# Optimization experiments

Hardware: AMD Instinct MI355X
Metric: run time of the kernel (lower is better)

The kernel has to match this reference:

```python
import jax, jax.numpy as jnp
import numpy as np

B, Nres, TOP_K, NUM_RBF = 2, 2048, 30, 16
MAX_REL = 32  # positional clip range -> 2*32+2 = 66 classes


def _gather_nodes(nodes, idx):
    # nodes: [B, N, ...], idx: [B, N, K] -> [B, N, K, ...]
    return jax.vmap(lambda n, i: n[i])(nodes, idx)


def _rbf(D):
    # D: [..., ] -> [..., NUM_RBF]; mu in [2, 22], sigma = 20/16
    mu = jnp.linspace(2.0, 22.0, NUM_RBF)
    sigma = (22.0 - 2.0) / NUM_RBF
    return jnp.exp(-(((D[..., None] - mu) / sigma) ** 2))


def setup_inputs() -> dict:
    key = jax.random.key(0)
    ks = jax.random.split(key, 4)
    X = jax.random.normal(ks[0], (B, Nres, 4, 3), dtype=jnp.float32) * 3.0
    mask = jnp.ones((B, Nres), dtype=jnp.float32)
    residue_idx = jnp.broadcast_to(jnp.arange(Nres, dtype=jnp.int32)[None], (B, Nres))
    chain_labels = jnp.zeros((B, Nres), dtype=jnp.int32)
    w_pos = jax.random.normal(ks[1], (66, 16), dtype=jnp.float32) * 0.05
    b_pos = jax.random.normal(ks[2], (16,), dtype=jnp.float32) * 0.05
    w_edge = jax.random.normal(ks[3], (416, 128), dtype=jnp.float32) * 0.05
    ln_gamma = jnp.ones((128,), dtype=jnp.float32)
    ln_beta = jnp.zeros((128,), dtype=jnp.float32)
    return dict(X=X, mask=mask, residue_idx=residue_idx, chain_labels=chain_labels,
                w_pos=w_pos, b_pos=b_pos, w_edge=w_edge, ln_gamma=ln_gamma, ln_beta=ln_beta)


def reference(X, mask, residue_idx, chain_labels, w_pos, b_pos, w_edge, ln_gamma, ln_beta):
    # virtual C-beta from N, C, Ca (atom order in X: N=0, C=1, Ca=2, O=3)
    b = X[:, :, 2, :] - X[:, :, 0, :]
    c = X[:, :, 1, :] - X[:, :, 2, :]
    a = jnp.cross(b, c)
    Cb = -0.58273431 * a + 0.56802827 * b - 0.54067466 * c + X[:, :, 2, :]
    N_, C, Ca, O = X[:, :, 0, :], X[:, :, 1, :], X[:, :, 2, :], X[:, :, 3, :]

    # masked kNN on C atoms (ProteinFeatures._dist)
    m2 = mask[:, None, :] * mask[:, :, None]                       # [B,N,N]
    dX = C[:, None, :, :] - C[:, :, None, :]
    D = m2 * jnp.sqrt(jnp.sum(dX ** 2, -1) + 1e-6)
    D_max = jnp.max(D, -1, keepdims=True)
    D_adj = D + (1.0 - m2) * D_max
    neg, E_idx = jax.lax.top_k(-D_adj, TOP_K)                      # smallest-k
    D_neighbors = -neg                                             # [B,N,K]

    # 25-channel RBF features; gather neighbor coords instead of NxN per pair
    atoms = jnp.stack([N_, Ca, Cb, C, O], 0)                       # [5,B,N,3]
    gathered = jax.vmap(lambda A: _gather_nodes(A, E_idx))(atoms)  # [5,B,N,K,3]
    # pair order follows torch source: NN,CaCa,CbCb,CN,CCa,CCb,NCa,NCb,CbCa,
    # NC,CaC,CbC,CaN,CbN,CaCb,OO,CO,OC,NO,ON,CbO,OCa,OCb,CaO  (0=N,1=Ca,2=Cb,3=C,4=O)
    pa = jnp.array([0, 1, 2, 3, 3, 3, 0, 0, 2, 0, 1, 2, 1, 2, 1, 4, 3, 4, 0, 4, 2, 4, 4, 1])
    pb = jnp.array([0, 1, 2, 0, 1, 2, 1, 2, 1, 3, 3, 3, 0, 0, 2, 4, 4, 3, 4, 0, 4, 1, 2, 4])
    A_sel = atoms[pa]                                              # [24,B,N,3]
    Bn_sel = gathered[pb]                                          # [24,B,N,K,3]
    Dp = jnp.sqrt(jnp.sum((A_sel[:, :, :, None, :] - Bn_sel) ** 2, -1) + 1e-6)
    RBF_all = jnp.concatenate([_rbf(D_neighbors)[None], _rbf(Dp)], 0)  # [25,B,N,K,16]
    RBF_all = jnp.moveaxis(RBF_all, 0, 3).reshape(B, Nres, TOP_K, 25 * NUM_RBF)

    # positional encodings over gathered offsets / chain match
    offset = residue_idx[:, :, None] - _gather_nodes(residue_idx, E_idx)   # [B,N,K]
    E_chains = (chain_labels[:, :, None] == _gather_nodes(chain_labels, E_idx)).astype(jnp.int32)
    d = jnp.clip(offset + MAX_REL, 0, 2 * MAX_REL) * E_chains + (1 - E_chains) * (2 * MAX_REL + 1)
    E_pos = w_pos[d] + b_pos                                       # one_hot @ W == gather

    # edge embedding + layernorm
    E = jnp.concatenate([E_pos, RBF_all], -1) @ w_edge             # [B,N,K,128]
    mu = E.mean(-1, keepdims=True)
    var = E.var(-1, keepdims=True)
    E = (E - mu) / jnp.sqrt(var + 1e-5) * ln_gamma + ln_beta
    return E, E_idx
```

## Files before the change

kernel.cpp:

```cpp
#include <hip/hip_runtime.h>
#include <hip/hip_bf16.h>
#include <stdint.h>

#define BB    2
#define NRES  2048
#define TOPK  30
#define NRBF  16
#define NFEAT 416
#define NCH   128
#define NKT   13

typedef __attribute__((ext_vector_type(8))) short bf16x8;
typedef __attribute__((ext_vector_type(4))) float f32x4;

__constant__ int c_pa[24] = {0,1,2,3,3,3,0,0,2,0,1,2,1,2,1,4,3,4,0,4,2,4,4,1};
__constant__ int c_pb[24] = {0,1,2,0,1,2,1,2,1,3,3,3,0,0,2,4,4,3,4,0,4,1,2,4};

static __device__ __forceinline__ unsigned short f2bf(float x) {
  __hip_bfloat16 h = __float2bfloat16(x);
  return *reinterpret_cast<unsigned short*>(&h);
}
static __device__ __forceinline__ unsigned pack2(float lo, float hi) {
  return (unsigned)f2bf(lo) | ((unsigned)f2bf(hi) << 16);
}

__global__ __launch_bounds__(256) void prep_kernel(const float* __restrict__ X,
                                                   const float* __restrict__ w_edge,
                                                   float* __restrict__ atoms,
                                                   float4* __restrict__ Cpk,
                                                   unsigned short* __restrict__ wB) {
  if (blockIdx.x < 16) {
    int id = blockIdx.x * 256 + threadIdx.x;
    const float* x = X + (size_t)id * 12;
    float nx = x[0], ny = x[1], nz = x[2];
    float cx = x[3], cy = x[4], cz = x[5];
    float ax = x[6], ay = x[7], az = x[8];
    float ox = x[9], oy = x[10], oz = x[11];
    float bx = ax - nx, by = ay - ny, bz = az - nz;
    float ccx = cx - ax, ccy = cy - ay, ccz = cz - az;
    float crx = by * ccz - bz * ccy;
    float cry = bz * ccx - bx * ccz;
    float crz = bx * ccy - by * ccx;
    float cbx = -0.58273431f * crx + 0.56802827f * bx - 0.54067466f * ccx + ax;
    float cby = -0.58273431f * cry + 0.56802827f * by - 0.54067466f * ccy + ay;
    float cbz = -0.58273431f * crz + 0.56802827f * bz - 0.54067466f * ccz + az;
    float* r = atoms + (size_t)id * 16;
    r[0] = nx;  r[1] = ny;  r[2] = nz;
    r[3] = ax;  r[4] = ay;  r[5] = az;
    r[6] = cbx; r[7] = cby; r[8] = cbz;
    r[9] = cx;  r[10] = cy; r[11] = cz;
    r[12] = ox; r[13] = oy; r[14] = oz;
    r[15] = 0.f;
    Cpk[id] = make_float4(cx, cy, cz, 0.f);
  } else {
    int id = (blockIdx.x - 16) * 256 + threadIdx.x;
    if (id >= NFEAT * NCH) return;
    int j    = id & 7;
    int lane = (id >> 3) & 63;
    int nt   = (id >> 9) & 7;
    int kt   = id >> 12;
    int col  = nt * 16 + (lane & 15);
    int k    = kt * 32 + ((lane >> 4) << 3) + j;
    wB[id] = f2bf(w_edge[(size_t)k * NCH + col]);
  }
}

__global__ __launch_bounds__(256) void topk_kernel(const float4* __restrict__ Cpk,
                                                   int* __restrict__ eidx,
                                                   float* __restrict__ dn,
                                                   float* __restrict__ outI) {
  int tid = threadIdx.x;
  int lane = tid & 63;
  int bi = blockIdx.x * 4 + (tid >> 6);
  int b = bi >> 11;
  int i = bi & (NRES - 1);
  const float4* Cb = Cpk + (size_t)b * NRES;
  float4 ci = Cb[i];

  unsigned long long key[4][8];
  unsigned long long sub[4];
#pragma unroll
  for (int g = 0; g < 4; ++g) {
    sub[g] = ~0ull;
#pragma unroll
    for (int s = 0; s < 8; ++s) {
      int j = lane + 64 * (g * 8 + s);
      float4 cj = Cb[j];
      float dx = cj.x - ci.x, dy = cj.y - ci.y, dz = cj.z - ci.z;
      float sm = __fadd_rn(__fadd_rn(__fadd_rn(__fmul_rn(dx, dx), __fmul_rn(dy, dy)),
                                     __fmul_rn(dz, dz)), 1e-6f);
      float d = sqrtf(sm);
      key[g][s] = ((unsigned long long)__float_as_uint(d) << 32) | (unsigned)j;
      if (key[g][s] < sub[g]) sub[g] = key[g][s];
    }
  }

  for (int k = 0; k < TOPK; ++k) {
    unsigned long long m01 = sub[0] < sub[1] ? sub[0] : sub[1];
    unsigned long long m23 = sub[2] < sub[3] ? sub[2] : sub[3];
    unsigned long long gm = m01 < m23 ? m01 : m23;
#pragma unroll
    for (int off = 32; off; off >>= 1) {
      unsigned long long o = __shfl_xor(gm, off, 64);
      if (o < gm) gm = o;
    }
    if (lane == 0) {
      int idx = (int)(unsigned)(gm & 0xffffffffu);
      eidx[(size_t)bi * TOPK + k] = idx;
      dn[(size_t)bi * TOPK + k] = __uint_as_float((unsigned)(gm >> 32));
      outI[(size_t)bi * TOPK + k] = (float)idx;
    }
#pragma unroll
    for (int g = 0; g < 4; ++g) {
      if (sub[g] == gm) {
        sub[g] = ~0ull;
#pragma unroll
        for (int s = 0; s < 8; ++s) {
          if (key[g][s] == gm) key[g][s] = ~0ull;
          if (key[g][s] < sub[g]) sub[g] = key[g][s];
        }
      }
    }
  }
}

__global__ __launch_bounds__(256) void edge_mfma_kernel(
    const float* __restrict__ atoms, const int* __restrict__ eidx_g,
    const float* __restrict__ dn_g, const int* __restrict__ ridx,
    const int* __restrict__ chain, const float* __restrict__ w_pos,
    const float* __restrict__ b_pos, const unsigned short* __restrict__ wB,
    const float* __restrict__ gamma, const float* __restrict__ beta,
    float* __restrict__ outE) {
  __shared__ __align__(16) unsigned fa[NKT * 4 * 32 * 4];
  __shared__ float nat[TOPK][16];
  __shared__ float iat[16];
  __shared__ float dn_s[TOPK];
  __shared__ int   dsel[TOPK];
  __shared__ float2 lnp[32][4];

  int tid = threadIdx.x;
  int bi = blockIdx.x;
  int b = bi >> 11;

  if (tid < TOPK) {
    dn_s[tid] = dn_g[(size_t)bi * TOPK + tid];
    int j = eidx_g[(size_t)bi * TOPK + tid];
    int off = ridx[bi] - ridx[b * NRES + j];
    int ec = (chain[bi] == chain[b * NRES + j]) ? 1 : 0;
    int d = off + 32; d = d < 0 ? 0 : (d > 64 ? 64 : d);
    dsel[tid] = ec ? d : 65;
  }
  if (tid >= 64 && tid < 80) iat[tid - 64] = atoms[(size_t)bi * 16 + (tid - 64)];
  for (int idx = tid; idx < TOPK * 16; idx += 256) {
    int e = idx >> 4, f = idx & 15;
    nat[e][f] = atoms[((size_t)(b * NRES) + eidx_g[(size_t)bi * TOPK + e]) * 16 + f];
  }
  for (int idx = tid; idx < NKT * 4 * 2 * 4; idx += 256) {
    int kt4q = idx >> 3, row = 30 + ((idx >> 2) & 1), jw = idx & 3;
    fa[(kt4q * 32 + row) * 4 + jw] = 0u;
  }
  __syncthreads();

  if (tid < TOPK * 8) {
    int e = tid >> 3, u = tid & 7;
    int q = u >> 2, jw = u & 3;
    int f0 = u * 2, ds = dsel[e];
    float v0 = w_pos[ds * 16 + f0] + b_pos[f0];
    float v1 = w_pos[ds * 16 + f0 + 1] + b_pos[f0 + 1];
    fa[((q * 32) + e) * 4 + jw] = pack2(v0, v1);
  }
  for (int idx = tid; idx < TOPK * 25; idx += 256) {
    int e = idx / 25, g = idx - e * 25;
    float d;
    if (g == 0) {
      d = dn_s[e];
    } else {
      int qq = g - 1;
      const float* A  = &iat[c_pa[qq] * 3];
      const float* Bv = &nat[e][c_pb[qq] * 3];
      float dx = A[0] - Bv[0], dy = A[1] - Bv[1], dz = A[2] - Bv[2];
      d = sqrtf(dx * dx + dy * dy + dz * dz + 1e-6f);
    }
    unsigned tmp[8];
#pragma unroll
    for (int j = 0; j < 8; ++j) {
      float mu0 = 2.0f + (float)(2 * j) * (20.0f / 15.0f);
      float mu1 = 2.0f + (float)(2 * j + 1) * (20.0f / 15.0f);
      float t0 = (d - mu0) * 0.8f, t1 = (d - mu1) * 0.8f;
      tmp[j] = pack2(__expf(-t0 * t0), __expf(-t1 * t1));
    }
    int u0 = 8 + 8 * g;
    int kt = u0 >> 4, q0 = (u0 >> 2) & 3;
    unsigned* dst0 = &fa[(((kt * 4 + q0) * 32) + e) * 4];
    unsigned* dst1 = &fa[(((kt * 4 + q0 + 1) * 32) + e) * 4];
    *(uint4*)dst0 = make_uint4(tmp[0], tmp[1], tmp[2], tmp[3]);
    *(uint4*)dst1 = make_uint4(tmp[4], tmp[5], tmp[6], tmp[7]);
  }
  __syncthreads();

  int nq = tid >> 6, lane = tid & 63;
  int q = lane >> 4;
  int ccol = lane & 15;
  const uint4* faq = ((const uint4*)fa) + q * 32;
  const bf16x8* wBv = (const bf16x8*)wB;

  union AV { uint4 u4; bf16x8 v; };
  AV a0[2], a1[2];
  bf16x8 b0[3], b1[3];
#pragma unroll
  for (int t = 0; t < 3; ++t) {
    b0[t] = wBv[((size_t)(t * 8) + nq * 2 + 0) * 64 + lane];
    b1[t] = wBv[((size_t)(t * 8) + nq * 2 + 1) * 64 + lane];
  }
#pragma unroll
  for (int t = 0; t < 2; ++t) {
    a0[t].u4 = faq[t * 128 + ccol];
    a1[t].u4 = faq[t * 128 + 16 + ccol];
  }

  f32x4 acc00 = {}, acc01 = {}, acc10 = {}, acc11 = {};
#pragma unroll
  for (int kt = 0; kt < NKT; ++kt) {
    if (kt + 3 < NKT) {
      b0[(kt + 3) % 3] = wBv[((size_t)((kt + 3) * 8) + nq * 2 + 0) * 64 + lane];
      b1[(kt + 3) % 3] = wBv[((size_t)((kt + 3) * 8) + nq * 2 + 1) * 64 + lane];
    }
    if (kt + 2 < NKT) {
      a0[(kt + 2) & 1].u4 = faq[(kt + 2) * 128 + ccol];
      a1[(kt + 2) & 1].u4 = faq[(kt + 2) * 128 + 16 + ccol];
    }
    acc00 = __builtin_amdgcn_mfma_f32_16x16x32_bf16(a0[kt & 1].v, b0[kt % 3], acc00, 0, 0, 0);
    acc01 = __builtin_amdgcn_mfma_f32_16x16x32_bf16(a0[kt & 1].v, b1[kt % 3], acc01, 0, 0, 0);
    acc10 = __builtin_amdgcn_mfma_f32_16x16x32_bf16(a1[kt & 1].v, b0[kt % 3], acc10, 0, 0, 0);
    acc11 = __builtin_amdgcn_mfma_f32_16x16x32_bf16(a1[kt & 1].v, b1[kt % 3], acc11, 0, 0, 0);
  }

#pragma unroll
  for (int mh = 0; mh < 2; ++mh) {
#pragma unroll
    for (int reg = 0; reg < 4; ++reg) {
      float v0 = mh ? acc10[reg] : acc00[reg];
      float v1 = mh ? acc11[reg] : acc01[reg];
      float s = v0 + v1, ss = v0 * v0 + v1 * v1;
      s  += __shfl_xor(s, 1, 64);  ss += __shfl_xor(ss, 1, 64);
      s  += __shfl_xor(s, 2, 64);  ss += __shfl_xor(ss, 2, 64);
      s  += __shfl_xor(s, 4, 64);  ss += __shfl_xor(ss, 4, 64);
      s  += __shfl_xor(s, 8, 64);  ss += __shfl_xor(ss, 8, 64);
      if (ccol == 0) lnp[(mh << 4) + q * 4 + reg][nq] = make_float2(s, ss);
    }
  }
  __syncthreads();

  float g0 = gamma[(nq * 2 + 0) * 16 + ccol], be0 = beta[(nq * 2 + 0) * 16 + ccol];
  float g1 = gamma[(nq * 2 + 1) * 16 + ccol], be1 = beta[(nq * 2 + 1) * 16 + ccol];
#pragma unroll
  for (int mh = 0; mh < 2; ++mh) {
#pragma unroll
    for (int reg = 0; reg < 4; ++reg) {
      int m = (mh << 4) + q * 4 + reg;
      if (m < TOPK) {
        float2 p0 = lnp[m][0], p1 = lnp[m][1], p2 = lnp[m][2], p3 = lnp[m][3];
        float s = (p0.x + p1.x) + (p2.x + p3.x);
        float ss = (p0.y + p1.y) + (p2.y + p3.y);
        float mu = s * (1.0f / 128.0f);
        float var = ss * (1.0f / 128.0f) - mu * mu;
        float rstd = rsqrtf(var + 1e-5f);
        float va = mh ? acc10[reg] : acc00[reg];
        float vb = mh ? acc11[reg] : acc01[reg];
        float* o = outE + ((size_t)bi * TOPK + m) * NCH + ccol;
        o[(nq * 2 + 0) * 16] = (va - mu) * rstd * g0 + be0;
        o[(nq * 2 + 1) * 16] = (vb - mu) * rstd * g1 + be1;
      }
    }
  }
}

extern "C" void kernel_launch(void* const* d_in, const int* in_sizes, int n_in,
                              void* d_out, int out_size, void* d_ws, size_t ws_size,
                              hipStream_t stream) {
  const float* X      = (const float*)d_in[0];
  const int*   ridx   = (const int*)d_in[2];
  const int*   chain  = (const int*)d_in[3];
  const float* w_pos  = (const float*)d_in[4];
  const float* b_pos  = (const float*)d_in[5];
  const float* w_edge = (const float*)d_in[6];
  const float* gamma  = (const float*)d_in[7];
  const float* beta   = (const float*)d_in[8];

  float* outE = (float*)d_out;
  float* outI = outE + (size_t)BB * NRES * TOPK * NCH;

  char* p = (char*)d_ws;
  float* atoms = (float*)p;                 p += (size_t)BB * NRES * 16 * 4;
  int*   eidx  = (int*)p;                   p += (size_t)BB * NRES * TOPK * 4;
  float* dn    = (float*)p;                 p += (size_t)BB * NRES * TOPK * 4;
  unsigned short* wB = (unsigned short*)p;  p += (size_t)NCH * NFEAT * 2;
  float4* Cpk  = (float4*)p;

  prep_kernel<<<16 + (NFEAT * NCH + 255) / 256, 256, 0, stream>>>(X, w_edge, atoms, Cpk, wB);
  topk_kernel<<<BB * NRES / 4, 256, 0, stream>>>(Cpk, eidx, dn, outI);
  edge_mfma_kernel<<<BB * NRES, 256, 0, stream>>>(atoms, eidx, dn, ridx, chain,
                                                  w_pos, b_pos, wB, gamma, beta, outE);
}
```

Baseline: 83.61 us.

## Switch edge embedding GEMM from bf16 to fp8 MFMA with row-major feature layout

Converts the edge-feature operands and the packed w_edge weights to FP8 (via cvt_pk_fp8) and uses the 16x16x32 fp8 MFMA instead of bf16. The shared feature buffer changes to a row-major layout with a padded stride, and the manual register prefetch pipeline is removed. This halves the weight and feature bytes and the packing work, at a real cost in precision: FP8 quantization of RBF values and weights could push outputs past the tolerance.

Measured after the change: 77.38 us. -7.4%, faster.

```diff
diff --git a/kernel.cpp b/kernel.cpp
--- a/kernel.cpp
+++ b/kernel.cpp
@@ -8,27 +8,27 @@
 #define NRBF  16
 #define NFEAT 416
 #define NCH   128
+#define NS8   108
 #define NKT   13
 
-typedef __attribute__((ext_vector_type(8))) short bf16x8;
 typedef __attribute__((ext_vector_type(4))) float f32x4;
+typedef unsigned long long u64;
 
 __constant__ int c_pa[24] = {0,1,2,3,3,3,0,0,2,0,1,2,1,2,1,4,3,4,0,4,2,4,4,1};
 __constant__ int c_pb[24] = {0,1,2,0,1,2,1,2,1,3,3,3,0,0,2,4,4,3,4,0,4,1,2,4};
 
-static __device__ __forceinline__ unsigned short f2bf(float x) {
-  __hip_bfloat16 h = __float2bfloat16(x);
-  return *reinterpret_cast<unsigned short*>(&h);
-}
-static __device__ __forceinline__ unsigned pack2(float lo, float hi) {
-  return (unsigned)f2bf(lo) | ((unsigned)f2bf(hi) << 16);
+static __device__ __forceinline__ unsigned pack4_fp8(float f0, float f1, float f2, float f3) {
+  unsigned r = 0;
+  r = __builtin_amdgcn_cvt_pk_fp8_f32(f0, f1, r, false);
+  r = __builtin_amdgcn_cvt_pk_fp8_f32(f2, f3, r, true);
+  return r;
 }
 
 __global__ __launch_bounds__(256) void prep_kernel(const float* __restrict__ X,
                                                    const float* __restrict__ w_edge,
                                                    float* __restrict__ atoms,
                                                    float4* __restrict__ Cpk,
-                                                   unsigned short* __restrict__ wB) {
+                                                   unsigned* __restrict__ wB8) {
   if (blockIdx.x < 16) {
     int id = blockIdx.x * 256 + threadIdx.x;
     const float* x = X + (size_t)id * 12;
@@ -54,14 +54,19 @@
     Cpk[id] = make_float4(cx, cy, cz, 0.f);
   } else {
     int id = (blockIdx.x - 16) * 256 + threadIdx.x;
-    if (id >= NFEAT * NCH) return;
-    int j    = id & 7;
-    int lane = (id >> 3) & 63;
-    int nt   = (id >> 9) & 7;
-    int kt   = id >> 12;
+    if (id >= NFEAT * NCH / 4) return;
+    int bb   = id * 4;
+    int j0   = bb & 7;
+    int lane = (bb >> 3) & 63;
+    int nt   = (bb >> 9) & 7;
+    int kt   = bb >> 12;
     int col  = nt * 16 + (lane & 15);
-    int k    = kt * 32 + ((lane >> 4) << 3) + j;
-    wB[id] = f2bf(w_edge[(size_t)k * NCH + col]);
+    int kb   = kt * 32 + ((lane >> 4) << 3) + j0;
+    float f0 = w_edge[(size_t)(kb + 0) * NCH + col];
+    float f1 = w_edge[(size_t)(kb + 1) * NCH + col];
+    float f2 = w_edge[(size_t)(kb + 2) * NCH + col];
+    float f3 = w_edge[(size_t)(kb + 3) * NCH + col];
+    wB8[id] = pack4_fp8(f0, f1, f2, f3);
   }
 }
 
@@ -77,8 +82,8 @@
   const float4* Cb = Cpk + (size_t)b * NRES;
   float4 ci = Cb[i];
 
-  unsigned long long key[4][8];
-  unsigned long long sub[4];
+  u64 key[4][8];
+  u64 sub[4];
 #pragma unroll
   for (int g = 0; g < 4; ++g) {
     sub[g] = ~0ull;
@@ -90,18 +95,18 @@
       float sm = __fadd_rn(__fadd_rn(__fadd_rn(__fmul_rn(dx, dx), __fmul_rn(dy, dy)),
                                      __fmul_rn(dz, dz)), 1e-6f);
       float d = sqrtf(sm);
-      key[g][s] = ((unsigned long long)__float_as_uint(d) << 32) | (unsigned)j;
+      key[g][s] = ((u64)__float_as_uint(d) << 32) | (unsigned)j;
       if (key[g][s] < sub[g]) sub[g] = key[g][s];
     }
   }
 
   for (int k = 0; k < TOPK; ++k) {
-    unsigned long long m01 = sub[0] < sub[1] ? sub[0] : sub[1];
-    unsigned long long m23 = sub[2] < sub[3] ? sub[2] : sub[3];
-    unsigned long long gm = m01 < m23 ? m01 : m23;
+    u64 m01 = sub[0] < sub[1] ? sub[0] : sub[1];
+    u64 m23 = sub[2] < sub[3] ? sub[2] : sub[3];
+    u64 gm = m01 < m23 ? m01 : m23;
 #pragma unroll
     for (int off = 32; off; off >>= 1) {
-      unsigned long long o = __shfl_xor(gm, off, 64);
+      u64 o = __shfl_xor(gm, off, 64);
       if (o < gm) gm = o;
     }
     if (lane == 0) {
@@ -128,10 +133,10 @@
     const float* __restrict__ atoms, const int* __restrict__ eidx_g,
     const float* __restrict__ dn_g, const int* __restrict__ ridx,
     const int* __restrict__ chain, const float* __restrict__ w_pos,
-    const float* __restrict__ b_pos, const unsigned short* __restrict__ wB,
+    const float* __restrict__ b_pos, const unsigned* __restrict__ wB8,
     const float* __restrict__ gamma, const float* __restrict__ beta,
     float* __restrict__ outE) {
-  __shared__ __align__(16) unsigned fa[NKT * 4 * 32 * 4];
+  __shared__ __align__(16) unsigned feat8[32 * NS8];
   __shared__ float nat[TOPK][16];
   __shared__ float iat[16];
   __shared__ float dn_s[TOPK];
@@ -141,6 +146,8 @@
   int tid = threadIdx.x;
   int bi = blockIdx.x;
   int b = bi >> 11;
+  int nq = tid >> 6, lane = tid & 63;
+  int q = lane >> 4, ccol = lane & 15;
 
   if (tid < TOPK) {
     dn_s[tid] = dn_g[(size_t)bi * TOPK + tid];
@@ -155,19 +162,17 @@
     int e = idx >> 4, f = idx & 15;
     nat[e][f] = atoms[((size_t)(b * NRES) + eidx_g[(size_t)bi * TOPK + e]) * 16 + f];
   }
-  for (int idx = tid; idx < NKT * 4 * 2 * 4; idx += 256) {
-    int kt4q = idx >> 3, row = 30 + ((idx >> 2) & 1), jw = idx & 3;
-    fa[(kt4q * 32 + row) * 4 + jw] = 0u;
-  }
+  for (int idx = tid; idx < 2 * NS8; idx += 256)
+    feat8[30 * NS8 + idx] = 0u;
   __syncthreads();
 
-  if (tid < TOPK * 8) {
-    int e = tid >> 3, u = tid & 7;
-    int q = u >> 2, jw = u & 3;
-    int f0 = u * 2, ds = dsel[e];
-    float v0 = w_pos[ds * 16 + f0] + b_pos[f0];
-    float v1 = w_pos[ds * 16 + f0 + 1] + b_pos[f0 + 1];
-    fa[((q * 32) + e) * 4 + jw] = pack2(v0, v1);
+  if (tid < TOPK * 4) {
+    int e = tid >> 2, p = tid & 3;
+    int f0 = p * 4, ds = dsel[e];
+    feat8[e * NS8 + p] = pack4_fp8(w_pos[ds * 16 + f0 + 0] + b_pos[f0 + 0],
+                                   w_pos[ds * 16 + f0 + 1] + b_pos[f0 + 1],
+                                   w_pos[ds * 16 + f0 + 2] + b_pos[f0 + 2],
+                                   w_pos[ds * 16 + f0 + 3] + b_pos[f0 + 3]);
   }
   for (int idx = tid; idx < TOPK * 25; idx += 256) {
     int e = idx / 25, g = idx - e * 25;
@@ -181,58 +186,38 @@
       float dx = A[0] - Bv[0], dy = A[1] - Bv[1], dz = A[2] - Bv[2];
       d = sqrtf(dx * dx + dy * dy + dz * dz + 1e-6f);
     }
-    unsigned tmp[8];
-#pragma unroll
-    for (int j = 0; j < 8; ++j) {
-      float mu0 = 2.0f + (float)(2 * j) * (20.0f / 15.0f);
-      float mu1 = 2.0f + (float)(2 * j + 1) * (20.0f / 15.0f);
-      float t0 = (d - mu0) * 0.8f, t1 = (d - mu1) * 0.8f;
-      tmp[j] = pack2(__expf(-t0 * t0), __expf(-t1 * t1));
-    }
-    int u0 = 8 + 8 * g;
-    int kt = u0 >> 4, q0 = (u0 >> 2) & 3;
-    unsigned* dst0 = &fa[(((kt * 4 + q0) * 32) + e) * 4];
-    unsigned* dst1 = &fa[(((kt * 4 + q0 + 1) * 32) + e) * 4];
-    *(uint4*)dst0 = make_uint4(tmp[0], tmp[1], tmp[2], tmp[3]);
-    *(uint4*)dst1 = make_uint4(tmp[4], tmp[5], tmp[6], tmp[7]);
+    float v[16];
+#pragma unroll
+    for (int j = 0; j < 16; ++j) {
+      float mu = 2.0f + (float)j * (20.0f / 15.0f);
+      float t = (d - mu) * 0.8f;
+      v[j] = __expf(-t * t);
+    }
+    uint4 w4 = make_uint4(pack4_fp8(v[0], v[1], v[2], v[3]),
+                          pack4_fp8(v[4], v[5], v[6], v[7]),
+                          pack4_fp8(v[8], v[9], v[10], v[11]),
+                          pack4_fp8(v[12], v[13], v[14], v[15]));
+    *(uint4*)&feat8[e * NS8 + 4 + 4 * g] = w4;
   }
   __syncthreads();
 
-  int nq = tid >> 6, lane = tid & 63;
-  int q = lane >> 4;
-  int ccol = lane & 15;
-  const uint4* faq = ((const uint4*)fa) + q * 32;
-  const bf16x8* wBv = (const bf16x8*)wB;
-
-  union AV { uint4 u4; bf16x8 v; };
-  AV a0[2], a1[2];
-  bf16x8 b0[3], b1[3];
-#pragma unroll
-  for (int t = 0; t < 3; ++t) {
-    b0[t] = wBv[((size_t)(t * 8) + nq * 2 + 0) * 64 + lane];
-    b1[t] = wBv[((size_t)(t * 8) + nq * 2 + 1) * 64 + lane];
-  }
-#pragma unroll
-  for (int t = 0; t < 2; ++t) {
-    a0[t].u4 = faq[t * 128 + ccol];
-    a1[t].u4 = faq[t * 128 + 16 + ccol];
-  }
+  const unsigned* ar0 = &feat8[ccol * NS8];
+  const unsigned* ar1 = &feat8[(16 + ccol) * NS8];
+  const u64* wBll = (const u64*)wB8;
 
   f32x4 acc00 = {}, acc01 = {}, acc10 = {}, acc11 = {};
 #pragma unroll
   for (int kt = 0; kt < NKT; ++kt) {
-    if (kt + 3 < NKT) {
-      b0[(kt + 3) % 3] = wBv[((size_t)((kt + 3) * 8) + nq * 2 + 0) * 64 + lane];
-      b1[(kt + 3) % 3] = wBv[((size_t)((kt + 3) * 8) + nq * 2 + 1) * 64 + lane];
-    }
-    if (kt + 2 < NKT) {
-      a0[(kt + 2) & 1].u4 = faq[(kt + 2) * 128 + ccol];
-      a1[(kt + 2) & 1].u4 = faq[(kt + 2) * 128 + 16 + ccol];
-    }
-    acc00 = __builtin_amdgcn_mfma_f32_16x16x32_bf16(a0[kt & 1].v, b0[kt % 3], acc00, 0, 0, 0);
-    acc01 = __builtin_amdgcn_mfma_f32_16x16x32_bf16(a0[kt & 1].v, b1[kt % 3], acc01, 0, 0, 0);
-    acc10 = __builtin_amdgcn_mfma_f32_16x16x32_bf16(a1[kt & 1].v, b0[kt % 3], acc10, 0, 0, 0);
-    acc11 = __builtin_amdgcn_mfma_f32_16x16x32_bf16(a1[kt & 1].v, b1[kt % 3], acc11, 0, 0, 0);
+    union { unsigned u[2]; long long l; } a0, a1;
+    int ao = kt * 8 + q * 2;
+    a0.u[0] = ar0[ao]; a0.u[1] = ar0[ao + 1];
+    a1.u[0] = ar1[ao]; a1.u[1] = ar1[ao + 1];
+    long long b0 = (long long)wBll[(size_t)(kt * 8 + nq * 2 + 0) * 64 + lane];
+    long long b1 = (long long)wBll[(size_t)(kt * 8 + nq * 2 + 1) * 64 + lane];
+    acc00 = __builtin_amdgcn_mfma_f32_16x16x32_fp8_fp8(a0.l, b0, acc00, 0, 0, 0);
+    acc01 = __builtin_amdgcn_mfma_f32_16x16x32_fp8_fp8(a0.l, b1, acc01, 0, 0, 0);
+    acc10 = __builtin_amdgcn_mfma_f32_16x16x32_fp8_fp8(a1.l, b0, acc10, 0, 0, 0);
+    acc11 = __builtin_amdgcn_mfma_f32_16x16x32_fp8_fp8(a1.l, b1, acc11, 0, 0, 0);
   }
 
 #pragma unroll
@@ -294,11 +279,11 @@
   float* atoms = (float*)p;                 p += (size_t)BB * NRES * 16 * 4;
   int*   eidx  = (int*)p;                   p += (size_t)BB * NRES * TOPK * 4;
   float* dn    = (float*)p;                 p += (size_t)BB * NRES * TOPK * 4;
-  unsigned short* wB = (unsigned short*)p;  p += (size_t)NCH * NFEAT * 2;
+  unsigned* wB8 = (unsigned*)p;             p += (size_t)NCH * NFEAT;
   float4* Cpk  = (float4*)p;
 
-  prep_kernel<<<16 + (NFEAT * NCH + 255) / 256, 256, 0, stream>>>(X, w_edge, atoms, Cpk, wB);
+  prep_kernel<<<16 + (NFEAT * NCH / 4 + 255) / 256, 256, 0, stream>>>(X, w_edge, atoms, Cpk, wB8);
   topk_kernel<<<BB * NRES / 4, 256, 0, stream>>>(Cpk, eidx, dn, outI);
   edge_mfma_kernel<<<BB * NRES, 256, 0, stream>>>(atoms, eidx, dn, ridx, chain,
-                                                  w_pos, b_pos, wB, gamma, beta, outE);
-}
+                                                  w_pos, b_pos, wB8, gamma, beta, outE);
+}
```
